# Performance work log

Hardware: AMD Instinct MI355X
Metric: run time of the kernel (lower is better)

Reference implementation:

```python
import jax, jax.numpy as jnp
import numpy as np

N, D, E = 10000, 64, 32768   # nodes, padded degree, target edges
F, H, O = 64, 256, 1         # in_channels, hidden_channels, out_channels


def _linear_init(key, fin, fout):
    kw, kb = jax.random.split(key)
    s = 1.0 / np.sqrt(fin)
    w = jax.random.uniform(kw, (fin, fout), jnp.float32, -s, s)
    b = jax.random.uniform(kb, (fout,), jnp.float32, -s, s)
    return w, b


def setup_inputs() -> dict:
    key = jax.random.key(0)
    ks = jax.random.split(key, 12)
    x = jax.random.normal(ks[0], (N, F), jnp.float32)
    adj_nbr = jax.random.randint(ks[1], (N, D), 0, N)          # padded neighbor lists
    tar_ei = jax.random.randint(ks[2], (2, E), 0, N)           # target edges
    xcn_w1, xcn_b1 = _linear_init(ks[3], F, H)
    xcn_w2, xcn_b2 = _linear_init(ks[4], H, H)
    xcn_w3, xcn_b3 = _linear_init(ks[5], H, H)
    xij_w1, xij_b1 = _linear_init(ks[6], F, H)
    xij_w2, xij_b2 = _linear_init(ks[7], H, H)
    lin_w1, lin_b1 = _linear_init(ks[8], H, H)
    lin_w2, lin_b2 = _linear_init(ks[9], H, O)
    beta = jnp.ones((1,), jnp.float32)
    return dict(x=x, adj_nbr=adj_nbr, tar_ei=tar_ei, beta=beta,
                xcn_w1=xcn_w1, xcn_b1=xcn_b1, xcn_w2=xcn_w2, xcn_b2=xcn_b2,
                xcn_w3=xcn_w3, xcn_b3=xcn_b3,
                xij_w1=xij_w1, xij_b1=xij_b1, xij_w2=xij_w2, xij_b2=xij_b2,
                lin_w1=lin_w1, lin_b1=lin_b1, lin_w2=lin_w2, lin_b2=lin_b2)


def reference(x, adj_nbr, tar_ei, beta,
              xcn_w1, xcn_b1, xcn_w2, xcn_b2, xcn_w3, xcn_b3,
              xij_w1, xij_b1, xij_w2, xij_b2,
              lin_w1, lin_b1, lin_w2, lin_b2):
    relu = jax.nn.relu
    i, j = tar_ei[0], tar_ei[1]
    # adjoverlap: common-neighbor intersection of rows i and j of the adjacency
    ni = adj_nbr[i]                                   # [E, D] neighbors of i
    nj = adj_nbr[j]                                   # [E, D] neighbors of j
    cm = (ni[:, :, None] == nj[:, None, :]).any(-1)   # [E, D] ni[a] in N(j)?
    # spmm_add(cn, x): sum features of common neighbors per target edge
    xcn = jnp.einsum('ed,edf->ef', cm.astype(x.dtype), x[ni])  # [E, F]
    # xijlin(xi * xj): Linear -> ReLU -> Linear
    xij = x[i] * x[j]
    h_ij = relu(xij @ xij_w1 + xij_b1) @ xij_w2 + xij_b2
    # xcnlin(xcn): Linear -> ReLU -> Linear -> ReLU -> Linear
    h_cn = relu(xcn @ xcn_w1 + xcn_b1)
    h_cn = relu(h_cn @ xcn_w2 + xcn_b2)
    h_cn = h_cn @ xcn_w3 + xcn_b3
    # lin(xcnlin(xcn) * beta + xij): Linear -> ReLU -> Linear
    h = relu((h_cn * beta + h_ij) @ lin_w1 + lin_b1)
    return h @ lin_w2 + lin_b2                        # [E, O]
```

## Files before the change

### kernel.cpp

```cpp
#include <hip/hip_runtime.h>

#define NNODES 10000
#define DDEG   64
#define NEDGES 32768
#define FIN    64
#define HID    256

typedef __attribute__((ext_vector_type(8))) __bf16 bf16x8;
typedef __attribute__((ext_vector_type(4))) float  f32x4;

__device__ __forceinline__ unsigned short f2bf(float f) {
    unsigned x = __float_as_uint(f);
    return (unsigned short)((x + 0x7FFFu + ((x >> 16) & 1u)) >> 16);
}
__device__ __forceinline__ float b2f(unsigned short u) {
    return __uint_as_float(((unsigned)u) << 16);
}

#define OFF_XIJ1 0
#define OFF_XIJ2 16384
#define OFF_XCN1 81920
#define OFF_XCN2 98304
#define OFF_XCN3 163840
#define OFF_LIN1 229376
#define WT_TOTAL 294912
#define NTILES   36

__host__ __device__ constexpr int tile_off(int t) {
    return t < 2  ? OFF_XIJ1 + t * 8192
         : t < 10 ? OFF_XIJ2 + (t - 2) * 8192
         : t < 12 ? OFF_XCN1 + (t - 10) * 8192
         : t < 20 ? OFF_XCN2 + (t - 12) * 8192
         : t < 28 ? OFF_XCN3 + (t - 20) * 8192
         :          OFF_LIN1 + (t - 28) * 8192;
}

__device__ __forceinline__ void gll16(const unsigned short* g, unsigned short* l) {
    __builtin_amdgcn_global_load_lds(
        (const __attribute__((address_space(1))) unsigned int*)g,
        (__attribute__((address_space(3))) unsigned int*)l, 16, 0, 0);
}
__device__ __forceinline__ void stage_act(const unsigned short* g, unsigned short* l,
                                          int tid, int wv) {
#pragma unroll
    for (int c = 0; c < 2; ++c)
        gll16(g + c * 2048 + tid * 8, l + c * 2048 + wv * 512);
}

__global__ __launch_bounds__(256) void edge_prep_k(const float* __restrict__ x,
                                                   const int* __restrict__ adj,
                                                   const int* __restrict__ tar,
                                                   const float* __restrict__ xij_w1,
                                                   const float* __restrict__ xij_w2,
                                                   const float* __restrict__ xcn_w1,
                                                   const float* __restrict__ xcn_w2,
                                                   const float* __restrict__ xcn_w3,
                                                   const float* __restrict__ lin_w1,
                                                   unsigned short* __restrict__ WT,
                                                   unsigned short* __restrict__ xij_g,
                                                   unsigned short* __restrict__ xcn_g) {
    const int wv   = threadIdx.x >> 6;
    const int lane = threadIdx.x & 63;
    const int e    = blockIdx.x * 4 + wv;

    int i = tar[e];
    int j = tar[NEDGES + e];
    int ni = adj[i * DDEG + lane];
    int nj = adj[j * DDEG + lane];
    float xi = x[i * FIN + lane];
    float xj = x[j * FIN + lane];

    bool found = false;
#pragma unroll
    for (int b = 0; b < 64; ++b)
        found |= (ni == (int)__builtin_amdgcn_readlane(nj, b));
    unsigned long long m = __ballot(found);

    float acc = 0.f;
    while (m) {
        int a = __ffsll(m) - 1;
        m &= m - 1;
        int r = (int)__builtin_amdgcn_readlane(ni, a);
        acc += x[r * FIN + lane];
    }
    int sl = lane ^ ((e & 7) << 3);
    xij_g[(size_t)e * FIN + sl] = f2bf(xi * xj);
    xcn_g[(size_t)e * FIN + sl] = f2bf(acc);

    if (blockIdx.x < WT_TOTAL / 256) {
        int idx = blockIdx.x * 256 + threadIdx.x;
        const float* src;
        int r;
        if (idx < OFF_XIJ2)      { r = idx - OFF_XIJ1; src = xij_w1; }
        else if (idx < OFF_XCN1) { r = idx - OFF_XIJ2; src = xij_w2; }
        else if (idx < OFF_XCN2) { r = idx - OFF_XCN1; src = xcn_w1; }
        else if (idx < OFF_XCN3) { r = idx - OFF_XCN2; src = xcn_w2; }
        else if (idx < OFF_LIN1) { r = idx - OFF_XCN3; src = xcn_w3; }
        else                     { r = idx - OFF_LIN1; src = lin_w1; }
        int kb  = r >> 13;
        int n   = (r & 8191) >> 5;
        int klo = r & 31;
        WT[idx] = f2bf(src[(kb * 32 + klo) * HID + n]);
    }
}

template <int T0, int NT, int LDA>
__device__ __forceinline__ void run_phase(const unsigned short* As,
                                          const unsigned short* __restrict__ WT,
                                          int boff, int lr, int lg,
                                          bf16x8 (&bq)[4][4], f32x4 acc[4][4]) {
#pragma unroll
    for (int m = 0; m < 4; ++m)
#pragma unroll
        for (int n = 0; n < 4; ++n) acc[m][n] = (f32x4){0.f, 0.f, 0.f, 0.f};
    const int sw = (lr & 7) << 3;
#pragma unroll
    for (int s = 0; s < NT; ++s) {
        const int t = T0 + s;
        bf16x8 a[4];
#pragma unroll
        for (int m = 0; m < 4; ++m)
            a[m] = *reinterpret_cast<const bf16x8*>(
                &As[(m * 16 + lr) * LDA + ((s * 32 + 8 * lg) ^ sw)]);
        __builtin_amdgcn_s_setprio(1);
#pragma unroll
        for (int m = 0; m < 4; ++m)
#pragma unroll
            for (int n = 0; n < 4; ++n)
                acc[m][n] = __builtin_amdgcn_mfma_f32_16x16x32_bf16(a[m], bq[t & 3][n], acc[m][n], 0, 0, 0);
        __builtin_amdgcn_s_setprio(0);
        if (t + 4 < NTILES) {
#pragma unroll
            for (int n = 0; n < 4; ++n)
                bq[(t + 4) & 3][n] = *reinterpret_cast<const bf16x8*>(
                    &WT[tile_off(t + 4) + boff + n * 512]);
        }
    }
}

__device__ __forceinline__ void fence_barrier() {
    asm volatile("s_waitcnt lgkmcnt(0)" ::: "memory");
    __builtin_amdgcn_s_barrier();
}

__global__ __launch_bounds__(256, 2) void mlp_k(const unsigned short* __restrict__ xij_g,
                                                const unsigned short* __restrict__ xcn_g,
                                                const unsigned short* __restrict__ WT,
                                                unsigned* __restrict__ hij_g,
                                                const float* __restrict__ xij_b1,
                                                const float* __restrict__ xij_b2,
                                                const float* __restrict__ xcn_b1,
                                                const float* __restrict__ xcn_b2,
                                                const float* __restrict__ xcn_b3,
                                                const float* __restrict__ lin_b1,
                                                const float* __restrict__ lin_w2,
                                                const float* __restrict__ lin_b2,
                                                const float* __restrict__ beta,
                                                float* __restrict__ out) {
    __shared__ unsigned short sXij[64 * 64];
    __shared__ unsigned short sXcn[64 * 64];
    __shared__ unsigned short sH[64 * 256];

    const int tid  = threadIdx.x;
    const int wv   = tid >> 6;
    const int lane = tid & 63;
    const int lr   = lane & 15;
    const int lg   = lane >> 4;
    const int col0 = wv * 64;
    const int row0 = blockIdx.x * 64;
    const int boff = (col0 + lr) * 32 + 8 * lg;

    stage_act(xij_g + (size_t)row0 * FIN, sXij, tid, wv);
    stage_act(xcn_g + (size_t)row0 * FIN, sXcn, tid, wv);
    bf16x8 bq[4][4];
#pragma unroll
    for (int t = 0; t < 4; ++t)
#pragma unroll
        for (int n = 0; n < 4; ++n)
            bq[t][n] = *reinterpret_cast<const bf16x8*>(&WT[tile_off(t) + boff + n * 512]);
    const float betaf = beta[0];
    unsigned* hbase = hij_g + (size_t)(blockIdx.x * 4 + wv) * 2048 + lane * 2;
    asm volatile("s_waitcnt vmcnt(16)" ::: "memory");
    __builtin_amdgcn_s_barrier();

    f32x4 acc[4][4];
    float bl[4];

    run_phase<0, 2, 64>(sXij, WT, boff, lr, lg, bq, acc);
#pragma unroll
    for (int n = 0; n < 4; ++n) bl[n] = xij_b1[col0 + n * 16 + lr];
#pragma unroll
    for (int m = 0; m < 4; ++m)
#pragma unroll
        for (int n = 0; n < 4; ++n)
#pragma unroll
            for (int i = 0; i < 4; ++i) {
                int row = m * 16 + 4 * lg + i;
                int col = col0 + n * 16 + lr;
                sH[row * HID + (col ^ ((row & 7) << 3))] = f2bf(fmaxf(acc[m][n][i] + bl[n], 0.f));
            }
    fence_barrier();

    run_phase<2, 8, 256>(sH, WT, boff, lr, lg, bq, acc);
#pragma unroll
    for (int n = 0; n < 4; ++n) bl[n] = xij_b2[col0 + n * 16 + lr];
#pragma unroll
    for (int m = 0; m < 4; ++m)
#pragma unroll
        for (int n = 0; n < 4; ++n) {
            uint2 v;
            v.x = ((unsigned)f2bf(acc[m][n][1] + bl[n]) << 16) | f2bf(acc[m][n][0] + bl[n]);
            v.y = ((unsigned)f2bf(acc[m][n][3] + bl[n]) << 16) | f2bf(acc[m][n][2] + bl[n]);
            *reinterpret_cast<uint2*>(hbase + (m * 4 + n) * 128) = v;
        }
    fence_barrier();

    run_phase<10, 2, 64>(sXcn, WT, boff, lr, lg, bq, acc);
#pragma unroll
    for (int n = 0; n < 4; ++n) bl[n] = xcn_b1[col0 + n * 16 + lr];
#pragma unroll
    for (int m = 0; m < 4; ++m)
#pragma unroll
        for (int n = 0; n < 4; ++n)
#pragma unroll
            for (int i = 0; i < 4; ++i) {
                int row = m * 16 + 4 * lg + i;
                int col = col0 + n * 16 + lr;
                sH[row * HID + (col ^ ((row & 7) << 3))] = f2bf(fmaxf(acc[m][n][i] + bl[n], 0.f));
            }
    fence_barrier();

    run_phase<12, 8, 256>(sH, WT, boff, lr, lg, bq, acc);
    fence_barrier();
#pragma unroll
    for (int n = 0; n < 4; ++n) bl[n] = xcn_b2[col0 + n * 16 + lr];
#pragma unroll
    for (int m = 0; m < 4; ++m)
#pragma unroll
        for (int n = 0; n < 4; ++n)
#pragma unroll
            for (int i = 0; i < 4; ++i) {
                int row = m * 16 + 4 * lg + i;
                int col = col0 + n * 16 + lr;
                sH[row * HID + (col ^ ((row & 7) << 3))] = f2bf(fmaxf(acc[m][n][i] + bl[n], 0.f));
            }
    fence_barrier();

    run_phase<20, 8, 256>(sH, WT, boff, lr, lg, bq, acc);
    fence_barrier();
#pragma unroll
    for (int n = 0; n < 4; ++n) bl[n] = xcn_b3[col0 + n * 16 + lr];
#pragma unroll
    for (int m = 0; m < 4; ++m)
#pragma unroll
        for (int n = 0; n < 4; ++n) {
            uint2 v = *reinterpret_cast<const uint2*>(hbase + (m * 4 + n) * 128);
            float h0 = b2f((unsigned short)(v.x & 0xFFFF));
            float h1 = b2f((unsigned short)(v.x >> 16));
            float h2 = b2f((unsigned short)(v.y & 0xFFFF));
            float h3 = b2f((unsigned short)(v.y >> 16));
            float v0 = (acc[m][n][0] + bl[n]) * betaf + h0;
            float v1 = (acc[m][n][1] + bl[n]) * betaf + h1;
            float v2 = (acc[m][n][2] + bl[n]) * betaf + h2;
            float v3 = (acc[m][n][3] + bl[n]) * betaf + h3;
            int rb = m * 16 + 4 * lg;
            int col = col0 + n * 16 + lr;
            sH[(rb + 0) * HID + (col ^ (((rb + 0) & 7) << 3))] = f2bf(v0);
            sH[(rb + 1) * HID + (col ^ (((rb + 1) & 7) << 3))] = f2bf(v1);
            sH[(rb + 2) * HID + (col ^ (((rb + 2) & 7) << 3))] = f2bf(v2);
            sH[(rb + 3) * HID + (col ^ (((rb + 3) & 7) << 3))] = f2bf(v3);
        }
    fence_barrier();

    run_phase<28, 8, 256>(sH, WT, boff, lr, lg, bq, acc);
#pragma unroll
    for (int n = 0; n < 4; ++n) bl[n] = lin_b1[col0 + n * 16 + lr];
    float w2l[4];
#pragma unroll
    for (int n = 0; n < 4; ++n) w2l[n] = lin_w2[col0 + n * 16 + lr];
    float* sRed = (float*)sXij;
#pragma unroll
    for (int m = 0; m < 4; ++m) {
        float p[4] = {0.f, 0.f, 0.f, 0.f};
#pragma unroll
        for (int n = 0; n < 4; ++n)
#pragma unroll
            for (int i = 0; i < 4; ++i)
                p[i] += fmaxf(acc[m][n][i] + bl[n], 0.f) * w2l[n];
#pragma unroll
        for (int i = 0; i < 4; ++i) {
            float s = p[i];
            s += __shfl_xor(s, 1);
            s += __shfl_xor(s, 2);
            s += __shfl_xor(s, 4);
            s += __shfl_xor(s, 8);
            if (lr == 0) sRed[wv * 64 + m * 16 + 4 * lg + i] = s;
        }
    }
    __syncthreads();
    if (tid < 64)
        out[row0 + tid] = sRed[tid] + sRed[64 + tid] + sRed[128 + tid] + sRed[192 + tid] + lin_b2[0];
}

extern "C" void kernel_launch(void* const* d_in, const int* in_sizes, int n_in,
                              void* d_out, int out_size, void* d_ws, size_t ws_size,
                              hipStream_t stream) {
    const float* x      = (const float*)d_in[0];
    const int*   adj    = (const int*)d_in[1];
    const int*   tar    = (const int*)d_in[2];
    const float* beta   = (const float*)d_in[3];
    const float* xcn_w1 = (const float*)d_in[4];
    const float* xcn_b1 = (const float*)d_in[5];
    const float* xcn_w2 = (const float*)d_in[6];
    const float* xcn_b2 = (const float*)d_in[7];
    const float* xcn_w3 = (const float*)d_in[8];
    const float* xcn_b3 = (const float*)d_in[9];
    const float* xij_w1 = (const float*)d_in[10];
    const float* xij_b1 = (const float*)d_in[11];
    const float* xij_w2 = (const float*)d_in[12];
    const float* xij_b2 = (const float*)d_in[13];
    const float* lin_w1 = (const float*)d_in[14];
    const float* lin_b1 = (const float*)d_in[15];
    const float* lin_w2 = (const float*)d_in[16];
    const float* lin_b2 = (const float*)d_in[17];

    unsigned short* WT    = (unsigned short*)d_ws;
    unsigned short* xij_g = (unsigned short*)((char*)d_ws + 589824);
    unsigned short* xcn_g = (unsigned short*)((char*)d_ws + 4784128);
    unsigned*       hij_g = (unsigned*)((char*)d_ws + 8978432);

    edge_prep_k<<<NEDGES / 4, 256, 0, stream>>>(x, adj, tar,
                                                xij_w1, xij_w2, xcn_w1, xcn_w2, xcn_w3, lin_w1,
                                                WT, xij_g, xcn_g);
    mlp_k<<<NEDGES / 64, 256, 0, stream>>>(xij_g, xcn_g, WT, hij_g,
                                           xij_b1, xij_b2, xcn_b1, xcn_b2, xcn_b3,
                                           lin_b1, lin_w2, lin_b2, beta, (float*)d_out);
}
```

Before: 58.34 us.

## Double MLP row tile to 128 edges and keep h_ij in registers

The fused MLP kernel now processes 128 edges per block instead of 64, so each weight fragment loaded from global memory feeds twice as many MFMAs. The h_ij intermediate is held in registers across phases instead of round-tripping through a global scratch buffer. The cost is more registers (acc doubles to 8x4 f32x4 plus 64 packed h_ij words) and more LDS per block, with launch bounds lowered to one block per SIMD group. The grid is halved to 256 blocks, which may underfill the GPU's compute units.

```diff
diff --git a/kernel.cpp b/kernel.cpp
--- a/kernel.cpp
+++ b/kernel.cpp
@@ -40,10 +40,10 @@
         (const __attribute__((address_space(1))) unsigned int*)g,
         (__attribute__((address_space(3))) unsigned int*)l, 16, 0, 0);
 }
-__device__ __forceinline__ void stage_act(const unsigned short* g, unsigned short* l,
-                                          int tid, int wv) {
-#pragma unroll
-    for (int c = 0; c < 2; ++c)
+__device__ __forceinline__ void stage_act16(const unsigned short* g, unsigned short* l,
+                                            int tid, int wv) {
+#pragma unroll
+    for (int c = 0; c < 4; ++c)
         gll16(g + c * 2048 + tid * 8, l + c * 2048 + wv * 512);
 }
 
@@ -108,26 +108,26 @@
 __device__ __forceinline__ void run_phase(const unsigned short* As,
                                           const unsigned short* __restrict__ WT,
                                           int boff, int lr, int lg,
-                                          bf16x8 (&bq)[4][4], f32x4 acc[4][4]) {
-#pragma unroll
-    for (int m = 0; m < 4; ++m)
-#pragma unroll
-        for (int n = 0; n < 4; ++n) acc[m][n] = (f32x4){0.f, 0.f, 0.f, 0.f};
+                                          bf16x8 (&bq)[4][4], f32x4 acc[8][4]) {
+#pragma unroll
+    for (int mm = 0; mm < 8; ++mm)
+#pragma unroll
+        for (int n = 0; n < 4; ++n) acc[mm][n] = (f32x4){0.f, 0.f, 0.f, 0.f};
     const int sw = (lr & 7) << 3;
 #pragma unroll
     for (int s = 0; s < NT; ++s) {
         const int t = T0 + s;
-        bf16x8 a[4];
-#pragma unroll
-        for (int m = 0; m < 4; ++m)
-            a[m] = *reinterpret_cast<const bf16x8*>(
-                &As[(m * 16 + lr) * LDA + ((s * 32 + 8 * lg) ^ sw)]);
+        bf16x8 a[8];
+#pragma unroll
+        for (int mm = 0; mm < 8; ++mm)
+            a[mm] = *reinterpret_cast<const bf16x8*>(
+                &As[(mm * 16 + lr) * LDA + ((s * 32 + 8 * lg) ^ sw)]);
         __builtin_amdgcn_s_setprio(1);
 #pragma unroll
-        for (int m = 0; m < 4; ++m)
+        for (int mm = 0; mm < 8; ++mm)
 #pragma unroll
             for (int n = 0; n < 4; ++n)
-                acc[m][n] = __builtin_amdgcn_mfma_f32_16x16x32_bf16(a[m], bq[t & 3][n], acc[m][n], 0, 0, 0);
+                acc[mm][n] = __builtin_amdgcn_mfma_f32_16x16x32_bf16(a[mm], bq[t & 3][n], acc[mm][n], 0, 0, 0);
         __builtin_amdgcn_s_setprio(0);
         if (t + 4 < NTILES) {
 #pragma unroll
@@ -143,10 +143,9 @@
     __builtin_amdgcn_s_barrier();
 }
 
-__global__ __launch_bounds__(256, 2) void mlp_k(const unsigned short* __restrict__ xij_g,
+__global__ __launch_bounds__(256, 1) void mlp_k(const unsigned short* __restrict__ xij_g,
                                                 const unsigned short* __restrict__ xcn_g,
                                                 const unsigned short* __restrict__ WT,
-                                                unsigned* __restrict__ hij_g,
                                                 const float* __restrict__ xij_b1,
                                                 const float* __restrict__ xij_b2,
                                                 const float* __restrict__ xcn_b1,
@@ -157,9 +156,9 @@
                                                 const float* __restrict__ lin_b2,
                                                 const float* __restrict__ beta,
                                                 float* __restrict__ out) {
-    __shared__ unsigned short sXij[64 * 64];
-    __shared__ unsigned short sXcn[64 * 64];
-    __shared__ unsigned short sH[64 * 256];
+    __shared__ unsigned short sXij[128 * 64];
+    __shared__ unsigned short sXcn[128 * 64];
+    __shared__ unsigned short sH[128 * 256];
 
     const int tid  = threadIdx.x;
     const int wv   = tid >> 6;
@@ -167,11 +166,11 @@
     const int lr   = lane & 15;
     const int lg   = lane >> 4;
     const int col0 = wv * 64;
-    const int row0 = blockIdx.x * 64;
+    const int row0 = blockIdx.x * 128;
     const int boff = (col0 + lr) * 32 + 8 * lg;
 
-    stage_act(xij_g + (size_t)row0 * FIN, sXij, tid, wv);
-    stage_act(xcn_g + (size_t)row0 * FIN, sXcn, tid, wv);
+    stage_act16(xij_g + (size_t)row0 * FIN, sXij, tid, wv);
+    stage_act16(xcn_g + (size_t)row0 * FIN, sXcn, tid, wv);
     bf16x8 bq[4][4];
 #pragma unroll
     for (int t = 0; t < 4; ++t)
@@ -179,39 +178,37 @@
         for (int n = 0; n < 4; ++n)
             bq[t][n] = *reinterpret_cast<const bf16x8*>(&WT[tile_off(t) + boff + n * 512]);
     const float betaf = beta[0];
-    unsigned* hbase = hij_g + (size_t)(blockIdx.x * 4 + wv) * 2048 + lane * 2;
     asm volatile("s_waitcnt vmcnt(16)" ::: "memory");
     __builtin_amdgcn_s_barrier();
 
-    f32x4 acc[4][4];
+    f32x4 acc[8][4];
     float bl[4];
 
     run_phase<0, 2, 64>(sXij, WT, boff, lr, lg, bq, acc);
 #pragma unroll
     for (int n = 0; n < 4; ++n) bl[n] = xij_b1[col0 + n * 16 + lr];
 #pragma unroll
-    for (int m = 0; m < 4; ++m)
+    for (int mm = 0; mm < 8; ++mm)
 #pragma unroll
         for (int n = 0; n < 4; ++n)
 #pragma unroll
             for (int i = 0; i < 4; ++i) {
-                int row = m * 16 + 4 * lg + i;
+                int row = mm * 16 + 4 * lg + i;
                 int col = col0 + n * 16 + lr;
-                sH[row * HID + (col ^ ((row & 7) << 3))] = f2bf(fmaxf(acc[m][n][i] + bl[n], 0.f));
+                sH[row * HID + (col ^ ((row & 7) << 3))] = f2bf(fmaxf(acc[mm][n][i] + bl[n], 0.f));
             }
     fence_barrier();
 
     run_phase<2, 8, 256>(sH, WT, boff, lr, lg, bq, acc);
 #pragma unroll
     for (int n = 0; n < 4; ++n) bl[n] = xij_b2[col0 + n * 16 + lr];
-#pragma unroll
-    for (int m = 0; m < 4; ++m)
+    unsigned hij_lo[8][4], hij_hi[8][4];
+#pragma unroll
+    for (int mm = 0; mm < 8; ++mm)
 #pragma unroll
         for (int n = 0; n < 4; ++n) {
-            uint2 v;
-            v.x = ((unsigned)f2bf(acc[m][n][1] + bl[n]) << 16) | f2bf(acc[m][n][0] + bl[n]);
-            v.y = ((unsigned)f2bf(acc[m][n][3] + bl[n]) << 16) | f2bf(acc[m][n][2] + bl[n]);
-            *reinterpret_cast<uint2*>(hbase + (m * 4 + n) * 128) = v;
+            hij_lo[mm][n] = ((unsigned)f2bf(acc[mm][n][1] + bl[n]) << 16) | f2bf(acc[mm][n][0] + bl[n]);
+            hij_hi[mm][n] = ((unsigned)f2bf(acc[mm][n][3] + bl[n]) << 16) | f2bf(acc[mm][n][2] + bl[n]);
         }
     fence_barrier();
 
@@ -219,14 +216,14 @@
 #pragma unroll
     for (int n = 0; n < 4; ++n) bl[n] = xcn_b1[col0 + n * 16 + lr];
 #pragma unroll
-    for (int m = 0; m < 4; ++m)
+    for (int mm = 0; mm < 8; ++mm)
 #pragma unroll
         for (int n = 0; n < 4; ++n)
 #pragma unroll
             for (int i = 0; i < 4; ++i) {
-                int row = m * 16 + 4 * lg + i;
+                int row = mm * 16 + 4 * lg + i;
                 int col = col0 + n * 16 + lr;
-                sH[row * HID + (col ^ ((row & 7) << 3))] = f2bf(fmaxf(acc[m][n][i] + bl[n], 0.f));
+                sH[row * HID + (col ^ ((row & 7) << 3))] = f2bf(fmaxf(acc[mm][n][i] + bl[n], 0.f));
             }
     fence_barrier();
 
@@ -235,14 +232,14 @@
 #pragma unroll
     for (int n = 0; n < 4; ++n) bl[n] = xcn_b2[col0 + n * 16 + lr];
 #pragma unroll
-    for (int m = 0; m < 4; ++m)
+    for (int mm = 0; mm < 8; ++mm)
 #pragma unroll
         for (int n = 0; n < 4; ++n)
 #pragma unroll
             for (int i = 0; i < 4; ++i) {
-                int row = m * 16 + 4 * lg + i;
+                int row = mm * 16 + 4 * lg + i;
                 int col = col0 + n * 16 + lr;
-                sH[row * HID + (col ^ ((row & 7) << 3))] = f2bf(fmaxf(acc[m][n][i] + bl[n], 0.f));
+                sH[row * HID + (col ^ ((row & 7) << 3))] = f2bf(fmaxf(acc[mm][n][i] + bl[n], 0.f));
             }
     fence_barrier();
 
@@ -251,19 +248,18 @@
 #pragma unroll
     for (int n = 0; n < 4; ++n) bl[n] = xcn_b3[col0 + n * 16 + lr];
 #pragma unroll
-    for (int m = 0; m < 4; ++m)
+    for (int mm = 0; mm < 8; ++mm)
 #pragma unroll
         for (int n = 0; n < 4; ++n) {
-            uint2 v = *reinterpret_cast<const uint2*>(hbase + (m * 4 + n) * 128);
-            float h0 = b2f((unsigned short)(v.x & 0xFFFF));
-            float h1 = b2f((unsigned short)(v.x >> 16));
-            float h2 = b2f((unsigned short)(v.y & 0xFFFF));
-            float h3 = b2f((unsigned short)(v.y >> 16));
-            float v0 = (acc[m][n][0] + bl[n]) * betaf + h0;
-            float v1 = (acc[m][n][1] + bl[n]) * betaf + h1;
-            float v2 = (acc[m][n][2] + bl[n]) * betaf + h2;
-            float v3 = (acc[m][n][3] + bl[n]) * betaf + h3;
-            int rb = m * 16 + 4 * lg;
+            float h0 = b2f((unsigned short)(hij_lo[mm][n] & 0xFFFF));
+            float h1 = b2f((unsigned short)(hij_lo[mm][n] >> 16));
+            float h2 = b2f((unsigned short)(hij_hi[mm][n] & 0xFFFF));
+            float h3 = b2f((unsigned short)(hij_hi[mm][n] >> 16));
+            float v0 = (acc[mm][n][0] + bl[n]) * betaf + h0;
+            float v1 = (acc[mm][n][1] + bl[n]) * betaf + h1;
+            float v2 = (acc[mm][n][2] + bl[n]) * betaf + h2;
+            float v3 = (acc[mm][n][3] + bl[n]) * betaf + h3;
+            int rb = mm * 16 + 4 * lg;
             int col = col0 + n * 16 + lr;
             sH[(rb + 0) * HID + (col ^ (((rb + 0) & 7) << 3))] = f2bf(v0);
             sH[(rb + 1) * HID + (col ^ (((rb + 1) & 7) << 3))] = f2bf(v1);
@@ -280,13 +276,13 @@
     for (int n = 0; n < 4; ++n) w2l[n] = lin_w2[col0 + n * 16 + lr];
     float* sRed = (float*)sXij;
 #pragma unroll
-    for (int m = 0; m < 4; ++m) {
+    for (int mm = 0; mm < 8; ++mm) {
         float p[4] = {0.f, 0.f, 0.f, 0.f};
 #pragma unroll
         for (int n = 0; n < 4; ++n)
 #pragma unroll
             for (int i = 0; i < 4; ++i)
-                p[i] += fmaxf(acc[m][n][i] + bl[n], 0.f) * w2l[n];
+                p[i] += fmaxf(acc[mm][n][i] + bl[n], 0.f) * w2l[n];
 #pragma unroll
         for (int i = 0; i < 4; ++i) {
             float s = p[i];
@@ -294,12 +290,12 @@
             s += __shfl_xor(s, 2);
             s += __shfl_xor(s, 4);
             s += __shfl_xor(s, 8);
-            if (lr == 0) sRed[wv * 64 + m * 16 + 4 * lg + i] = s;
+            if (lr == 0) sRed[wv * 128 + mm * 16 + 4 * lg + i] = s;
         }
     }
     __syncthreads();
-    if (tid < 64)
-        out[row0 + tid] = sRed[tid] + sRed[64 + tid] + sRed[128 + tid] + sRed[192 + tid] + lin_b2[0];
+    if (tid < 128)
+        out[row0 + tid] = sRed[tid] + sRed[128 + tid] + sRed[256 + tid] + sRed[384 + tid] + lin_b2[0];
 }
 
 extern "C" void kernel_launch(void* const* d_in, const int* in_sizes, int n_in,
@@ -327,12 +323,11 @@
     unsigned short* WT    = (unsigned short*)d_ws;
     unsigned short* xij_g = (unsigned short*)((char*)d_ws + 589824);
     unsigned short* xcn_g = (unsigned short*)((char*)d_ws + 4784128);
-    unsigned*       hij_g = (unsigned*)((char*)d_ws + 8978432);
 
     edge_prep_k<<<NEDGES / 4, 256, 0, stream>>>(x, adj, tar,
                                                 xij_w1, xij_w2, xcn_w1, xcn_w2, xcn_w3, lin_w1,
                                                 WT, xij_g, xcn_g);
-    mlp_k<<<NEDGES / 64, 256, 0, stream>>>(xij_g, xcn_g, WT, hij_g,
-                                           xij_b1, xij_b2, xcn_b1, xcn_b2, xcn_b3,
-                                           lin_b1, lin_w2, lin_b2, beta, (float*)d_out);
-}
+    mlp_k<<<NEDGES / 128, 256, 0, stream>>>(xij_g, xcn_g, WT,
+                                            xij_b1, xij_b2, xcn_b1, xcn_b2, xcn_b3,
+                                            lin_b1, lin_w2, lin_b2, beta, (float*)d_out);
+}
```

New measurement: 73.90 us. +26.7%, slower.
